# Performance work log

Measured on AMD Instinct MI355X. Metric: run time of the kernel, lower is better.

The kernel has to match this reference:

```python
import jax, jax.numpy as jnp
import numpy as np

B, T, E, D = 256, 128, 256, 256


def setup_inputs() -> dict:
    key = jax.random.key(0)
    ks = jax.random.split(key, 8)
    x = jax.random.normal(ks[0], (B, T, E), dtype=jnp.float32)
    # torch default Linear init: U(-1/sqrt(fan_in), 1/sqrt(fan_in)) for proj layers;
    # TreeLSTMCell.reset_parameters uses U(-1/sqrt(hidden), 1/sqrt(hidden)).
    se = 1.0 / np.sqrt(E)
    sd = 1.0 / np.sqrt(D)
    Wp = jax.random.uniform(ks[1], (E, D), jnp.float32, -se, se)
    bp = jax.random.uniform(ks[2], (D,), jnp.float32, -se, se)
    Wg = jax.random.uniform(ks[3], (E, D), jnp.float32, -se, se)
    bg = jax.random.uniform(ks[4], (D,), jnp.float32, -se, se)
    Wr = jax.random.uniform(ks[5], (2 * D, 5 * D), jnp.float32, -sd, sd)
    br = jax.random.uniform(ks[6], (5 * D,), jnp.float32, -sd, sd)
    # Valid shift-reduce sequence (right-branching): S, then (S, R) x (T-1) -> length 2T-1.
    pat = np.zeros(2 * T - 1, dtype=np.int32)
    pat[2::2] = 1  # REDUCE at odd stack-growth points
    transitions = jnp.asarray(np.broadcast_to(pat[:, None], (2 * T - 1, B)).copy())
    return {"x": x, "Wp": Wp, "bp": bp, "Wg": Wg, "bg": bg,
            "Wr": Wr, "br": br, "transitions": transitions}


def reference(x, Wp, bp, Wg, bg, Wr, br, transitions):
    Bx, Tx, _ = x.shape
    Dh = Wp.shape[1]
    # leaf transformation: c = Wx+b ; h = sigmoid(gate) * tanh(c)
    c_buf = x @ Wp + bp                                   # [B, T, D]
    h_buf = jax.nn.sigmoid(x @ Wg + bg) * jnp.tanh(c_buf)  # [B, T, D]
    buffers = jnp.concatenate([h_buf, c_buf], axis=-1)    # [B, T, 2D]

    stack0 = jnp.zeros((Bx, Tx, 2 * Dh), x.dtype)
    ptr0 = jnp.zeros((Bx,), jnp.int32)          # stack pointer (next free slot)
    bptr0 = jnp.full((Bx,), Tx - 1, jnp.int32)  # buffer pop index (pops from end)
    bidx = jnp.arange(Bx)

    def step(carry, trans_t):
        stack, ptr, bptr = carry
        is_shift = trans_t == 0
        shift_val = buffers[bidx, bptr]                       # [B, 2D]
        r = stack[bidx, jnp.maximum(ptr - 1, 0)]              # right child (top)
        l = stack[bidx, jnp.maximum(ptr - 2, 0)]              # left child
        h_l, c_l = l[:, :Dh], l[:, Dh:]
        h_r, c_r = r[:, :Dh], r[:, Dh:]
        proj = jnp.concatenate([h_l, h_r], axis=-1) @ Wr + br  # [B, 5D]
        i, f_l, f_r, g, o = jnp.split(proj, 5, axis=-1)
        c = (jax.nn.sigmoid(i) * jnp.tanh(g)
             + jax.nn.sigmoid(f_l) * c_l
             + jax.nn.sigmoid(f_r) * c_r)
        h = jax.nn.sigmoid(o) * jnp.tanh(c)
        red = jnp.concatenate([h, c], axis=-1)                # [B, 2D]
        pos = jnp.where(is_shift, ptr, jnp.maximum(ptr - 2, 0))
        val = jnp.where(is_shift[:, None], shift_val, red)
        stack = stack.at[bidx, pos].set(val)
        ptr = ptr + jnp.where(is_shift, jnp.int32(1), jnp.int32(-1))
        bptr = bptr - is_shift.astype(jnp.int32)
        return (stack, ptr, bptr), None

    (stack, ptr, _), _ = jax.lax.scan(step, (stack0, ptr0, bptr0), transitions)
    final = stack[bidx, jnp.maximum(ptr - 1, 0)][:, :Dh]  # root h states [B, D]
    return final
```

## Files before the change

kernel.cpp:

```cpp
#include <hip/hip_runtime.h>


typedef unsigned int u32;
typedef short s16x8 __attribute__((ext_vector_type(8)));
typedef float f32x4 __attribute__((ext_vector_type(4)));

#define MFMA16(a, b, c) __builtin_amdgcn_mfma_f32_16x16x32_bf16((a), (b), (c), 0, 0, 0)

static __device__ __forceinline__ unsigned short f2bf(float x) {
  u32 u = __builtin_bit_cast(u32, x);
  u += 0x7fffu + ((u >> 16) & 1u);
  return (unsigned short)(u >> 16);
}
static __device__ __forceinline__ float bf2f(unsigned short s) {
  u32 u = ((u32)s) << 16;
  return __builtin_bit_cast(float, u);
}
static __device__ __forceinline__ u32 packhl(float x) {
  unsigned short hi = f2bf(x);
  unsigned short lo = f2bf(x - bf2f(hi));
  return ((u32)hi << 16) | (u32)lo;
}
static __device__ __forceinline__ float unpackhl(u32 p) {
  return bf2f((unsigned short)(p >> 16)) + bf2f((unsigned short)(p & 0xffffu));
}
static __device__ __forceinline__ void unpack8(uint4 a, uint4 b, s16x8 &hi, s16x8 &lo) {
  hi[0] = (short)(a.x >> 16); lo[0] = (short)a.x;
  hi[1] = (short)(a.y >> 16); lo[1] = (short)a.y;
  hi[2] = (short)(a.z >> 16); lo[2] = (short)a.z;
  hi[3] = (short)(a.w >> 16); lo[3] = (short)a.w;
  hi[4] = (short)(b.x >> 16); lo[4] = (short)b.x;
  hi[5] = (short)(b.y >> 16); lo[5] = (short)b.y;
  hi[6] = (short)(b.z >> 16); lo[6] = (short)b.z;
  hi[7] = (short)(b.w >> 16); lo[7] = (short)b.w;
}
static __device__ __forceinline__ void split8(const float *w, s16x8 &hi, s16x8 &lo) {
#pragma unroll
  for (int i = 0; i < 8; i++) {
    unsigned short h = f2bf(w[i]);
    hi[i] = (short)h;
    lo[i] = (short)f2bf(w[i] - bf2f(h));
  }
}
static __device__ __forceinline__ float sigm(float x) { return 1.0f / (1.0f + expf(-x)); }
static __device__ __forceinline__ int vslot(int code) {
  return (code & 15) * 2 + ((code >> 4) & 1);
}

__global__ __launch_bounds__(256) void pack_kernel(
    const float *__restrict__ Wp, const float *__restrict__ Wg,
    const float *__restrict__ Wr, const float *__restrict__ x,
    u32 *__restrict__ Wpg_t, u32 *__restrict__ Wr_t, u32 *__restrict__ xpk,
    u32 *__restrict__ vstkH, float *__restrict__ vstkC, int do_x) {
  int tid = blockIdx.x * 256 + threadIdx.x;
  if (tid < 131072) {
    int isg = tid >= 65536;
    int s = tid & 65535;
    int k = s >> 8, col = s & 255;
    float v = isg ? Wg[s] : Wp[s];
    Wpg_t[(isg ? 256 + col : col) * 256 + k] = packhl(v);
  }
  if (tid < 655360) {
    int k = tid / 1280;
    int col = tid - k * 1280;
    Wr_t[col * 512 + k] = packhl(Wr[tid]);
  }
  if (tid < 65536) {
    vstkH[31 * 65536 + tid] = 0u;
    vstkC[31 * 65536 + tid] = 0.0f;
  }
  if (do_x && tid < 8388608) xpk[tid] = packhl(x[tid]);
}

__global__ __launch_bounds__(256) void plan_kernel(
    const int *__restrict__ trans, int *__restrict__ pL, int *__restrict__ pR,
    int *__restrict__ pW, int *__restrict__ fdesc) {
  int b = threadIdx.x;
  u32 t0 = 0x9F9F9F9Fu, t1 = t0, t2 = t0, t3 = t0;
  u32 verb = 0;
  int ptr = 0, bptr = 127;

  auto get = [&](int p) -> u32 {
    u32 w = p < 8 ? (p < 4 ? t0 : t1) : (p < 12 ? t2 : t3);
    return (w >> ((p & 3) * 8)) & 0xffu;
  };
  auto set = [&](int p, u32 e) {
    u32 sh = (u32)(p & 3) * 8u;
    u32 m = ~(0xffu << sh);
    u32 nv = e << sh;
    int ws = p >> 2;
    t0 = ws == 0 ? (t0 & m) | nv : t0;
    t1 = ws == 1 ? (t1 & m) | nv : t1;
    t2 = ws == 2 ? (t2 & m) | nv : t2;
    t3 = ws == 3 ? (t3 & m) | nv : t3;
  };
  auto dostep = [&](int tr, int &l, int &r, int &w) {
    if (tr == 0) {
      int pos = min(ptr, 15);
      set(pos, (u32)(bptr & 127));
      ptr++; bptr--;
    } else {
      int pl = min(max(ptr - 2, 0), 15);
      int pr = min(max(ptr - 1, 0), 15);
      l = (int)get(pl);
      r = (int)get(pr);
      u32 v = ((verb >> pl) & 1u) ^ 1u;
      verb = (verb & ~(1u << pl)) | (v << pl);
      set(pl, 0x80u | (v << 4) | (u32)pl);
      w = pl * 2 + (int)v;
      ptr--;
    }
  };
  auto ext = [&](int e) -> int { return (e & 0x80) ? (0x8000 | (e & 0x1f)) : e; };

  for (int f = 0; f < 128; ++f) {
    int l = 0x9F, r = 0x9F, w = -1;
    dostep(trans[(2 * f) * 256 + b], l, r, w);
    if (2 * f + 1 < 255) dostep(trans[(2 * f + 1) * 256 + b], l, r, w);
    pL[f * 256 + b] = ext(l);
    pR[f * 256 + b] = ext(r);
    pW[f * 256 + b] = w;
  }
  fdesc[b] = ext((int)get(min(max(ptr - 1, 0), 15)));
}

template <int UX>
__global__ __launch_bounds__(64) void front_kernel(
    const float *__restrict__ x, const u32 *__restrict__ xpk,
    const u32 *__restrict__ Wpg, const float *__restrict__ bp,
    const float *__restrict__ bg, u32 *__restrict__ h_buf,
    float *__restrict__ c_buf) {
  const int lane = threadIdx.x;
  const int rbase = blockIdx.x * 16;
  const int y = blockIdx.y;
  const int rlo = lane & 15;
  const int khi = (lane >> 4) * 8;

  f32x4 z = {0.f, 0.f, 0.f, 0.f};
  f32x4 aP[8], aG[8];
#pragma unroll
  for (int i = 0; i < 8; i++) { aP[i] = z; aG[i] = z; }

#pragma unroll 2
  for (int kt = 0; kt < 8; ++kt) {
    int k = kt * 32 + khi;
    s16x8 Ah, Al;
    if (UX) {
      const u32 *ap = xpk + (rbase + rlo) * 256 + k;
      uint4 a0 = *(const uint4 *)ap, a1 = *(const uint4 *)(ap + 4);
      unpack8(a0, a1, Ah, Al);
    } else {
      const float *ap = x + (rbase + rlo) * 256 + k;
      float4 v0 = *(const float4 *)ap;
      float4 v1 = *(const float4 *)(ap + 4);
      float w[8] = {v0.x, v0.y, v0.z, v0.w, v1.x, v1.y, v1.z, v1.w};
      split8(w, Ah, Al);
    }
#pragma unroll
    for (int nt = 0; nt < 8; ++nt) {
      int colP = y * 128 + nt * 16 + rlo;
      {
        const u32 *wp = Wpg + colP * 256 + k;
        uint4 q0 = *(const uint4 *)wp, q1 = *(const uint4 *)(wp + 4);
        s16x8 Bh, Bl;
        unpack8(q0, q1, Bh, Bl);
        aP[nt] = MFMA16(Ah, Bh, aP[nt]);
        aP[nt] = MFMA16(Ah, Bl, aP[nt]);
        aP[nt] = MFMA16(Al, Bh, aP[nt]);
      }
      {
        const u32 *wg = Wpg + (256 + colP) * 256 + k;
        uint4 q0 = *(const uint4 *)wg, q1 = *(const uint4 *)(wg + 4);
        s16x8 Bh, Bl;
        unpack8(q0, q1, Bh, Bl);
        aG[nt] = MFMA16(Ah, Bh, aG[nt]);
        aG[nt] = MFMA16(Ah, Bl, aG[nt]);
        aG[nt] = MFMA16(Al, Bh, aG[nt]);
      }
    }
  }
#pragma unroll
  for (int nt = 0; nt < 8; ++nt) {
    int d = y * 128 + nt * 16 + rlo;
    float bpd = bp[d], bgd = bg[d];
#pragma unroll
    for (int ri = 0; ri < 4; ++ri) {
      int r = rbase + (lane >> 4) * 4 + ri;
      float cv = aP[nt][ri] + bpd;
      float gv = aG[nt][ri] + bgd;
      c_buf[r * 256 + d] = cv;
      h_buf[r * 256 + d] = packhl(sigm(gv) * tanhf(cv));
    }
  }
}

#define KSTEP_BODY(SRC, KOFF)                                                \
  {                                                                          \
    const u32 *s = (SRC) + kt * 32 + khi;                                    \
    uint4 a0 = *(const uint4 *)s, a1 = *(const uint4 *)(s + 4);              \
    s16x8 Ah, Al;                                                            \
    unpack8(a0, a1, Ah, Al);                                                 \
    int kk = (KOFF) + kt * 32 + khi;                                         \
    {                                                                        \
      const u32 *wp = Wr_t + gcol0 * 512 + kk;                               \
      uint4 q0 = *(const uint4 *)wp, q1 = *(const uint4 *)(wp + 4);          \
      s16x8 Bh, Bl;                                                          \
      unpack8(q0, q1, Bh, Bl);                                               \
      acc0 = MFMA16(Ah, Bh, acc0);                                           \
      acc0 = MFMA16(Ah, Bl, acc0);                                           \
      acc0 = MFMA16(Al, Bh, acc0);                                           \
    }                                                                        \
    {                                                                        \
      const u32 *wp = Wr_t + gcol1 * 512 + kk;                               \
      uint4 q0 = *(const uint4 *)wp, q1 = *(const uint4 *)(wp + 4);          \
      s16x8 Bh, Bl;                                                          \
      unpack8(q0, q1, Bh, Bl);                                               \
      acc1 = MFMA16(Ah, Bh, acc1);                                           \
      acc1 = MFMA16(Ah, Bl, acc1);                                           \
      acc1 = MFMA16(Al, Bh, acc1);                                           \
    }                                                                        \
    {                                                                        \
      const u32 *wp = Wr_t + gcol2 * 512 + kk;                               \
      uint4 q0 = *(const uint4 *)wp, q1 = *(const uint4 *)(wp + 4);          \
      s16x8 Bh, Bl;                                                          \
      unpack8(q0, q1, Bh, Bl);                                               \
      acc2 = MFMA16(Ah, Bh, acc2);                                           \
      acc2 = MFMA16(Ah, Bl, acc2);                                           \
      acc2 = MFMA16(Al, Bh, acc2);                                           \
    }                                                                        \
  }

__global__ __launch_bounds__(64) void ppre_kernel(
    const float *__restrict__ br, const u32 *__restrict__ Wr_t,
    const u32 *__restrict__ h_buf, const u32 *__restrict__ vzero,
    const int *__restrict__ pL, const int *__restrict__ pR,
    const int *__restrict__ pW, float *__restrict__ ppre) {
  const int c = blockIdx.x;
  const int fl = blockIdx.y >> 4;
  const int g = blockIdx.y & 15;
  const int lane = threadIdx.x;
  const int b0 = g * 16;
  const int b = b0 + (lane & 15);

  const int lc = pL[fl * 256 + b];
  const int rc = pR[fl * 256 + b];
  const int w = pW[fl * 256 + b];
  if (__ballot(w >= 0) == 0ull) return;

  const bool lbuf = (lc & 0x8000) == 0;
  const bool rbuf = (rc & 0x8000) == 0;
  const u32 *srcT = lbuf ? h_buf + (((b << 7) + (lc & 127)) << 8) : vzero + (b << 8);
  const u32 *srcB = rbuf ? h_buf + (((b << 7) + (rc & 127)) << 8) : vzero + (b << 8);
  const bool doT = __ballot(w >= 0 && lbuf) != 0ull;
  const bool doB = __ballot(w >= 0 && rbuf) != 0ull;

  const int khi = (lane >> 4) * 8;
  const int cl = lane & 15;
  const int v2c = 32 + cl;
  const int gcol0 = (cl >> 3) * 256 + c * 8 + (cl & 7);
  const int gcol1 = ((16 + cl) >> 3) * 256 + c * 8 + (cl & 7);
  const int gcol2 = (v2c < 40) ? (v2c >> 3) * 256 + c * 8 + (v2c & 7) : 0;

  f32x4 acc0 = {0.f, 0.f, 0.f, 0.f}, acc1 = acc0, acc2 = acc0;
  if (doT) {
#pragma unroll 4
    for (int kt = 0; kt < 8; ++kt) KSTEP_BODY(srcT, 0)
  }
  if (doB) {
#pragma unroll 4
    for (int kt = 0; kt < 8; ++kt) KSTEP_BODY(srcB, 256)
  }

  int wcs[4];
#pragma unroll
  for (int ri = 0; ri < 4; ++ri) wcs[ri] = __shfl(w, (lane >> 4) * 4 + ri);
  float br0 = br[gcol0], br1 = br[gcol1], br2 = br[gcol2];
  float *pr = ppre + (size_t)fl * 327680;
#pragma unroll
  for (int ri = 0; ri < 4; ++ri) {
    if (wcs[ri] >= 0) {
      int b2 = b0 + (lane >> 4) * 4 + ri;
      float *row = pr + b2 * 1280;
      row[gcol0] = acc0[ri] + br0;
      row[gcol1] = acc1[ri] + br1;
      if (v2c < 40) row[gcol2] = acc2[ri] + br2;
    }
  }
}

template <int PPRE>
__global__ __launch_bounds__(64) void step_kernel(
    const float *__restrict__ br, const u32 *__restrict__ Wr_t,
    const u32 *__restrict__ h_buf, const float *__restrict__ c_buf,
    u32 *__restrict__ vstkH, float *__restrict__ vstkC,
    const u32 *__restrict__ vzero, const int *__restrict__ pL,
    const int *__restrict__ pR, const int *__restrict__ pW,
    const float *__restrict__ ppre) {
  const int c = blockIdx.x;
  const int g = blockIdx.y;
  const int lane = threadIdx.x;
  const int b0 = g * 16;
  const int b = b0 + (lane & 15);

  const int lc = pL[b];
  const int rc = pR[b];
  const int w = pW[b];
  if (__ballot(w >= 0) == 0ull) return;

  const bool lval = (lc & 0x8000) != 0;
  const bool rval = (rc & 0x8000) != 0;
  const u32 *srcT, *srcB;
  if (PPRE) {
    srcT = lval ? vstkH + ((vslot(lc) * 256 + b) << 8) : vzero + (b << 8);
    srcB = rval ? vstkH + ((vslot(rc) * 256 + b) << 8) : vzero + (b << 8);
  } else {
    srcT = lval ? vstkH + ((vslot(lc) * 256 + b) << 8)
                : h_buf + (((b << 7) + (lc & 127)) << 8);
    srcB = rval ? vstkH + ((vslot(rc) * 256 + b) << 8)
                : h_buf + (((b << 7) + (rc & 127)) << 8);
  }
  const bool doT = PPRE ? (__ballot(w >= 0 && lval) != 0ull) : true;
  const bool doB = PPRE ? (__ballot(w >= 0 && rval) != 0ull) : true;

  const int khi = (lane >> 4) * 8;
  const int cl = lane & 15;
  const int v2c = 32 + cl;
  const int gcol0 = (cl >> 3) * 256 + c * 8 + (cl & 7);
  const int gcol1 = ((16 + cl) >> 3) * 256 + c * 8 + (cl & 7);
  const int gcol2 = (v2c < 40) ? (v2c >> 3) * 256 + c * 8 + (v2c & 7) : 0;

  f32x4 acc0 = {0.f, 0.f, 0.f, 0.f}, acc1 = acc0, acc2 = acc0;
  if (doT) {
#pragma unroll 4
    for (int kt = 0; kt < 8; ++kt) KSTEP_BODY(srcT, 0)
  }
  if (doB) {
#pragma unroll 4
    for (int kt = 0; kt < 8; ++kt) KSTEP_BODY(srcB, 256)
  }

  f32x4 flv, gv;
#pragma unroll
  for (int ri = 0; ri < 4; ++ri) {
    flv[ri] = __shfl_xor(acc0[ri], 8);
    gv[ri] = __shfl_xor(acc1[ri], 8);
  }
  int lcs[4], rcs[4], wcs[4];
#pragma unroll
  for (int ri = 0; ri < 4; ++ri) {
    int rr = (lane >> 4) * 4 + ri;
    lcs[ri] = __shfl(lc, rr);
    rcs[ri] = __shfl(rc, rr);
    wcs[ri] = __shfl(w, rr);
  }
  int colj = lane & 15;
  if (colj < 8) {
    int d = c * 8 + colj;
    float brI = 0, brFl = 0, brFr = 0, brG = 0, brO = 0;
    if (!PPRE) {
      brI = br[d]; brFl = br[256 + d]; brFr = br[512 + d];
      brG = br[768 + d]; brO = br[1024 + d];
    }
#pragma unroll
    for (int ri = 0; ri < 4; ++ri) {
      if (wcs[ri] >= 0) {
        int b2 = b0 + (lane >> 4) * 4 + ri;
        int lc2 = lcs[ri], rc2 = rcs[ri];
        float c_l = (lc2 & 0x8000)
                        ? vstkC[(vslot(lc2) * 256 + b2) * 256 + d]
                        : c_buf[(b2 * 128 + (lc2 & 127)) * 256 + d];
        float c_r = (rc2 & 0x8000)
                        ? vstkC[(vslot(rc2) * 256 + b2) * 256 + d]
                        : c_buf[(b2 * 128 + (rc2 & 127)) * 256 + d];
        float pI, pFl, pFr, pG, pO;
        if (PPRE) {
          const float *row = ppre + (size_t)b2 * 1280;
          pI = row[d]; pFl = row[256 + d]; pFr = row[512 + d];
          pG = row[768 + d]; pO = row[1024 + d];
        } else {
          pI = brI; pFl = brFl; pFr = brFr; pG = brG; pO = brO;
        }
        float ii = acc0[ri] + pI;
        float fl = flv[ri] + pFl;
        float fr = acc1[ri] + pFr;
        float gg = gv[ri] + pG;
        float oo = acc2[ri] + pO;
        float cv = sigm(ii) * tanhf(gg) + sigm(fl) * c_l + sigm(fr) * c_r;
        float hv = sigm(oo) * tanhf(cv);
        int sidx = wcs[ri];
        vstkH[(sidx * 256 + b2) * 256 + d] = packhl(hv);
        vstkC[(sidx * 256 + b2) * 256 + d] = cv;
      }
    }
  }
}

__global__ __launch_bounds__(256) void out_kernel(
    const int *__restrict__ fdesc, const u32 *__restrict__ h_buf,
    const u32 *__restrict__ vstkH, float *__restrict__ out) {
  int tid = blockIdx.x * 256 + threadIdx.x;
  int b = tid >> 8, d = tid & 255;
  int code = fdesc[b];
  u32 hv = (code & 0x8000)
               ? vstkH[(vslot(code) * 256 + b) * 256 + d]
               : h_buf[(b * 128 + (code & 127)) * 256 + d];
  out[tid] = unpackhl(hv);
}

extern "C" void kernel_launch(void *const *d_in, const int *in_sizes, int n_in,
                              void *d_out, int out_size, void *d_ws, size_t ws_size,
                              hipStream_t stream) {
  const float *x = (const float *)d_in[0];
  const float *Wp = (const float *)d_in[1];
  const float *bp = (const float *)d_in[2];
  const float *Wg = (const float *)d_in[3];
  const float *bg = (const float *)d_in[4];
  const float *Wr = (const float *)d_in[5];
  const float *br = (const float *)d_in[6];
  const int *trans = (const int *)d_in[7];
  float *out = (float *)d_out;

  char *ws = (char *)d_ws;
  u32 *Wr_t = (u32 *)(ws);
  u32 *Wpg = (u32 *)(ws + 2621440);
  u32 *h_buf = (u32 *)(ws + 3145728);
  float *c_buf = (float *)(ws + 36700160);
  u32 *vstkH = (u32 *)(ws + 70254592);
  float *vstkC = (float *)(ws + 78643200);
  int *planL = (int *)(ws + 87031808);
  int *planR = (int *)(ws + 87162880);
  int *planW = (int *)(ws + 87293952);
  int *fdesc = (int *)(ws + 87425024);
  const u32 *vzero = vstkH + 31 * 65536;

  const size_t fixed_end = 87426048;
  const size_t slotB = 1310720;
  const size_t xpkB = 33554432;
  size_t avail = ws_size > fixed_end ? ws_size - fixed_end : 0;
  size_t tail = fixed_end;
  int use_xpk = 0;
  if (avail >= xpkB + 4 * slotB) { use_xpk = 1; tail += xpkB; avail -= xpkB; }
  u32 *xpk = (u32 *)(ws + fixed_end);
  int R = (int)(avail / slotB);
  if (R > 32) R = 32;
  R &= ~1;
  int use_ppre = (R >= 2);
  int C = use_ppre ? R / 2 : 0;
  float *ppre = (float *)(ws + tail);

  pack_kernel<<<use_xpk ? 32768 : 2560, 256, 0, stream>>>(
      Wp, Wg, Wr, x, Wpg, Wr_t, xpk, vstkH, vstkC, use_xpk);
  plan_kernel<<<1, 256, 0, stream>>>(trans, planL, planR, planW, fdesc);
  if (use_xpk)
    front_kernel<1><<<dim3(2048, 2), 64, 0, stream>>>(x, xpk, Wpg, bp, bg, h_buf, c_buf);
  else
    front_kernel<0><<<dim3(2048, 2), 64, 0, stream>>>(x, xpk, Wpg, bp, bg, h_buf, c_buf);

  if (use_ppre) {
    int nch = (128 + C - 1) / C;
    auto pre = [&](int k) {
      int f0 = k * C;
      int Ck = min(C, 128 - f0);
      ppre_kernel<<<dim3(32, Ck * 16), 64, 0, stream>>>(
          br, Wr_t, h_buf, vzero, planL + f0 * 256, planR + f0 * 256,
          planW + f0 * 256, ppre + (size_t)((k & 1) * C) * 327680);
    };
    pre(0);
    if (nch > 1) pre(1);
    for (int k = 0; k < nch; ++k) {
      int f0 = k * C;
      int Ck = min(C, 128 - f0);
      for (int fl = 0; fl < Ck; ++fl) {
        int f = f0 + fl;
        step_kernel<1><<<dim3(32, 16), 64, 0, stream>>>(
            br, Wr_t, h_buf, c_buf, vstkH, vstkC, vzero, planL + f * 256,
            planR + f * 256, planW + f * 256,
            ppre + (size_t)((k & 1) * C + fl) * 327680);
      }
      if (k + 2 < nch) pre(k + 2);
    }
  } else {
    for (int f = 0; f < 128; ++f)
      step_kernel<0><<<dim3(32, 16), 64, 0, stream>>>(
          br, Wr_t, h_buf, c_buf, vstkH, vstkC, vzero, planL + f * 256,
          planR + f * 256, planW + f * 256, nullptr);
  }
  out_kernel<<<256, 256, 0, stream>>>(fdesc, h_buf, vstkH, out);
}
```

Baseline: 2.249 ms.

## Replace per-step kernel launches with persistent scan kernel using group barriers

Replaces the 128 per-step kernel launches (plus chunked precompute kernels) with one persistent kernel of 512 workgroups. Each group of 32 workgroups sharing a batch slice synchronizes through an atomic counter barrier between steps. The ppre precompute of buffer-leaf projections and the packed-x path are removed, and the front kernel is split into 4 column groups instead of 2. This trades launch overhead and ppre traffic for spin-barrier latency and recomputing buffer-side matmuls inside the serial loop. It also relies on all 512 workgroups being co-resident to avoid deadlock.

```diff
diff --git a/kernel.cpp b/kernel.cpp
--- a/kernel.cpp
+++ b/kernel.cpp
@@ -4,6 +4,8 @@
 typedef unsigned int u32;
 typedef short s16x8 __attribute__((ext_vector_type(8)));
 typedef float f32x4 __attribute__((ext_vector_type(4)));
+
+#define NPAIR 128
 
 #define MFMA16(a, b, c) __builtin_amdgcn_mfma_f32_16x16x32_bf16((a), (b), (c), 0, 0, 0)
 
@@ -49,9 +51,9 @@
 
 __global__ __launch_bounds__(256) void pack_kernel(
     const float *__restrict__ Wp, const float *__restrict__ Wg,
-    const float *__restrict__ Wr, const float *__restrict__ x,
-    u32 *__restrict__ Wpg_t, u32 *__restrict__ Wr_t, u32 *__restrict__ xpk,
-    u32 *__restrict__ vstkH, float *__restrict__ vstkC, int do_x) {
+    const float *__restrict__ Wr, u32 *__restrict__ Wpg_t,
+    u32 *__restrict__ Wr_t, u32 *__restrict__ vstkH, float *__restrict__ vstkC,
+    u32 *__restrict__ bar, int do_bar) {
   int tid = blockIdx.x * 256 + threadIdx.x;
   if (tid < 131072) {
     int isg = tid >= 65536;
@@ -69,67 +71,73 @@
     vstkH[31 * 65536 + tid] = 0u;
     vstkC[31 * 65536 + tid] = 0.0f;
   }
-  if (do_x && tid < 8388608) xpk[tid] = packhl(x[tid]);
-}
+  if (do_bar && tid < 512) bar[tid] = 0u;
+}
+
+#define PGET(p, dst)                                                         \
+  {                                                                          \
+    u32 wsel = ((p) & 8) ? (((p) & 4) ? t3 : t2) : (((p) & 4) ? t1 : t0);    \
+    dst = (int)((wsel >> (((p) & 3) * 8)) & 0xffu);                          \
+  }
+#define PSET(p, e)                                                           \
+  {                                                                          \
+    u32 sh_ = (u32)((p) & 3) * 8u;                                           \
+    u32 m_ = ~(0xffu << sh_);                                                \
+    u32 nv_ = ((u32)(e)) << sh_;                                             \
+    int w_ = (p) >> 2;                                                       \
+    t0 = (w_ == 0) ? ((t0 & m_) | nv_) : t0;                                 \
+    t1 = (w_ == 1) ? ((t1 & m_) | nv_) : t1;                                 \
+    t2 = (w_ == 2) ? ((t2 & m_) | nv_) : t2;                                 \
+    t3 = (w_ == 3) ? ((t3 & m_) | nv_) : t3;                                 \
+  }
+#define PDOSTEP(tr, l, r, w)                                                 \
+  {                                                                          \
+    if ((tr) == 0) {                                                         \
+      int pos_ = min(ptr, 15);                                               \
+      PSET(pos_, (u32)(bptr & 127));                                         \
+      ptr++;                                                                 \
+      bptr--;                                                                \
+    } else {                                                                 \
+      int pl_ = min(max(ptr - 2, 0), 15);                                    \
+      int pr_ = min(max(ptr - 1, 0), 15);                                    \
+      PGET(pl_, l);                                                          \
+      PGET(pr_, r);                                                          \
+      u32 v_ = ((verb >> pl_) & 1u) ^ 1u;                                    \
+      verb = (verb & ~(1u << pl_)) | (v_ << pl_);                            \
+      PSET(pl_, 0x80u | (v_ << 4) | (u32)pl_);                               \
+      w = pl_ * 2 + (int)v_;                                                 \
+      ptr--;                                                                 \
+    }                                                                        \
+  }
 
 __global__ __launch_bounds__(256) void plan_kernel(
     const int *__restrict__ trans, int *__restrict__ pL, int *__restrict__ pR,
     int *__restrict__ pW, int *__restrict__ fdesc) {
   int b = threadIdx.x;
-  u32 t0 = 0x9F9F9F9Fu, t1 = t0, t2 = t0, t3 = t0;
+  u32 t0 = 0x9F9F9F9Fu, t1 = 0x9F9F9F9Fu, t2 = 0x9F9F9F9Fu, t3 = 0x9F9F9F9Fu;
   u32 verb = 0;
   int ptr = 0, bptr = 127;
 
-  auto get = [&](int p) -> u32 {
-    u32 w = p < 8 ? (p < 4 ? t0 : t1) : (p < 12 ? t2 : t3);
-    return (w >> ((p & 3) * 8)) & 0xffu;
-  };
-  auto set = [&](int p, u32 e) {
-    u32 sh = (u32)(p & 3) * 8u;
-    u32 m = ~(0xffu << sh);
-    u32 nv = e << sh;
-    int ws = p >> 2;
-    t0 = ws == 0 ? (t0 & m) | nv : t0;
-    t1 = ws == 1 ? (t1 & m) | nv : t1;
-    t2 = ws == 2 ? (t2 & m) | nv : t2;
-    t3 = ws == 3 ? (t3 & m) | nv : t3;
-  };
-  auto dostep = [&](int tr, int &l, int &r, int &w) {
-    if (tr == 0) {
-      int pos = min(ptr, 15);
-      set(pos, (u32)(bptr & 127));
-      ptr++; bptr--;
-    } else {
-      int pl = min(max(ptr - 2, 0), 15);
-      int pr = min(max(ptr - 1, 0), 15);
-      l = (int)get(pl);
-      r = (int)get(pr);
-      u32 v = ((verb >> pl) & 1u) ^ 1u;
-      verb = (verb & ~(1u << pl)) | (v << pl);
-      set(pl, 0x80u | (v << 4) | (u32)pl);
-      w = pl * 2 + (int)v;
-      ptr--;
-    }
-  };
-  auto ext = [&](int e) -> int { return (e & 0x80) ? (0x8000 | (e & 0x1f)) : e; };
-
-  for (int f = 0; f < 128; ++f) {
+  for (int f = 0; f < NPAIR; ++f) {
+    int trA = trans[(2 * f) * 256 + b];
+    int trB = (2 * f + 1 < 255) ? trans[(2 * f + 1) * 256 + b] : -1;
     int l = 0x9F, r = 0x9F, w = -1;
-    dostep(trans[(2 * f) * 256 + b], l, r, w);
-    if (2 * f + 1 < 255) dostep(trans[(2 * f + 1) * 256 + b], l, r, w);
-    pL[f * 256 + b] = ext(l);
-    pR[f * 256 + b] = ext(r);
+    PDOSTEP(trA, l, r, w);
+    if (trB >= 0) PDOSTEP(trB, l, r, w);
+    pL[f * 256 + b] = (l & 0x80) ? (0x8000 | (l & 0x1f)) : l;
+    pR[f * 256 + b] = (r & 0x80) ? (0x8000 | (r & 0x1f)) : r;
     pW[f * 256 + b] = w;
   }
-  fdesc[b] = ext((int)get(min(max(ptr - 1, 0), 15)));
-}
-
-template <int UX>
+  int pf = min(max(ptr - 1, 0), 15);
+  int fd;
+  PGET(pf, fd);
+  fdesc[b] = (fd & 0x80) ? (0x8000 | (fd & 0x1f)) : fd;
+}
+
 __global__ __launch_bounds__(64) void front_kernel(
-    const float *__restrict__ x, const u32 *__restrict__ xpk,
-    const u32 *__restrict__ Wpg, const float *__restrict__ bp,
-    const float *__restrict__ bg, u32 *__restrict__ h_buf,
-    float *__restrict__ c_buf) {
+    const float *__restrict__ x, const u32 *__restrict__ Wpg,
+    const float *__restrict__ bp, const float *__restrict__ bg,
+    u32 *__restrict__ h_buf, float *__restrict__ c_buf) {
   const int lane = threadIdx.x;
   const int rbase = blockIdx.x * 16;
   const int y = blockIdx.y;
@@ -137,19 +145,15 @@
   const int khi = (lane >> 4) * 8;
 
   f32x4 z = {0.f, 0.f, 0.f, 0.f};
-  f32x4 aP[8], aG[8];
-#pragma unroll
-  for (int i = 0; i < 8; i++) { aP[i] = z; aG[i] = z; }
+  f32x4 aP[4], aG[4];
+#pragma unroll
+  for (int i = 0; i < 4; i++) { aP[i] = z; aG[i] = z; }
 
 #pragma unroll 2
   for (int kt = 0; kt < 8; ++kt) {
     int k = kt * 32 + khi;
     s16x8 Ah, Al;
-    if (UX) {
-      const u32 *ap = xpk + (rbase + rlo) * 256 + k;
-      uint4 a0 = *(const uint4 *)ap, a1 = *(const uint4 *)(ap + 4);
-      unpack8(a0, a1, Ah, Al);
-    } else {
+    {
       const float *ap = x + (rbase + rlo) * 256 + k;
       float4 v0 = *(const float4 *)ap;
       float4 v1 = *(const float4 *)(ap + 4);
@@ -157,8 +161,8 @@
       split8(w, Ah, Al);
     }
 #pragma unroll
-    for (int nt = 0; nt < 8; ++nt) {
-      int colP = y * 128 + nt * 16 + rlo;
+    for (int nt = 0; nt < 4; ++nt) {
+      int colP = y * 64 + nt * 16 + rlo;
       {
         const u32 *wp = Wpg + colP * 256 + k;
         uint4 q0 = *(const uint4 *)wp, q1 = *(const uint4 *)(wp + 4);
@@ -180,8 +184,8 @@
     }
   }
 #pragma unroll
-  for (int nt = 0; nt < 8; ++nt) {
-    int d = y * 128 + nt * 16 + rlo;
+  for (int nt = 0; nt < 4; ++nt) {
+    int d = y * 64 + nt * 16 + rlo;
     float bpd = bp[d], bgd = bg[d];
 #pragma unroll
     for (int ri = 0; ri < 4; ++ri) {
@@ -230,29 +234,18 @@
     }                                                                        \
   }
 
-__global__ __launch_bounds__(64) void ppre_kernel(
-    const float *__restrict__ br, const u32 *__restrict__ Wr_t,
-    const u32 *__restrict__ h_buf, const u32 *__restrict__ vzero,
-    const int *__restrict__ pL, const int *__restrict__ pR,
-    const int *__restrict__ pW, float *__restrict__ ppre) {
-  const int c = blockIdx.x;
-  const int fl = blockIdx.y >> 4;
-  const int g = blockIdx.y & 15;
-  const int lane = threadIdx.x;
-  const int b0 = g * 16;
+static __device__ __forceinline__ void step_body(
+    int c, int b0, int lane, const float *__restrict__ br,
+    const u32 *__restrict__ Wr_t, const u32 *__restrict__ h_buf,
+    const float *__restrict__ c_buf, u32 *__restrict__ vstkH,
+    float *__restrict__ vstkC, int lc, int rc, int w) {
   const int b = b0 + (lane & 15);
-
-  const int lc = pL[fl * 256 + b];
-  const int rc = pR[fl * 256 + b];
-  const int w = pW[fl * 256 + b];
-  if (__ballot(w >= 0) == 0ull) return;
-
-  const bool lbuf = (lc & 0x8000) == 0;
-  const bool rbuf = (rc & 0x8000) == 0;
-  const u32 *srcT = lbuf ? h_buf + (((b << 7) + (lc & 127)) << 8) : vzero + (b << 8);
-  const u32 *srcB = rbuf ? h_buf + (((b << 7) + (rc & 127)) << 8) : vzero + (b << 8);
-  const bool doT = __ballot(w >= 0 && lbuf) != 0ull;
-  const bool doB = __ballot(w >= 0 && rbuf) != 0ull;
+  const bool lval = (lc & 0x8000) != 0;
+  const bool rval = (rc & 0x8000) != 0;
+  const u32 *srcT = lval ? vstkH + ((vslot(lc) * 256 + b) << 8)
+                         : h_buf + (((b << 7) + (lc & 127)) << 8);
+  const u32 *srcB = rval ? vstkH + ((vslot(rc) * 256 + b) << 8)
+                         : h_buf + (((b << 7) + (rc & 127)) << 8);
 
   const int khi = (lane >> 4) * 8;
   const int cl = lane & 15;
@@ -262,82 +255,10 @@
   const int gcol2 = (v2c < 40) ? (v2c >> 3) * 256 + c * 8 + (v2c & 7) : 0;
 
   f32x4 acc0 = {0.f, 0.f, 0.f, 0.f}, acc1 = acc0, acc2 = acc0;
-  if (doT) {
 #pragma unroll 4
-    for (int kt = 0; kt < 8; ++kt) KSTEP_BODY(srcT, 0)
-  }
-  if (doB) {
+  for (int kt = 0; kt < 8; ++kt) KSTEP_BODY(srcT, 0)
 #pragma unroll 4
-    for (int kt = 0; kt < 8; ++kt) KSTEP_BODY(srcB, 256)
-  }
-
-  int wcs[4];
-#pragma unroll
-  for (int ri = 0; ri < 4; ++ri) wcs[ri] = __shfl(w, (lane >> 4) * 4 + ri);
-  float br0 = br[gcol0], br1 = br[gcol1], br2 = br[gcol2];
-  float *pr = ppre + (size_t)fl * 327680;
-#pragma unroll
-  for (int ri = 0; ri < 4; ++ri) {
-    if (wcs[ri] >= 0) {
-      int b2 = b0 + (lane >> 4) * 4 + ri;
-      float *row = pr + b2 * 1280;
-      row[gcol0] = acc0[ri] + br0;
-      row[gcol1] = acc1[ri] + br1;
-      if (v2c < 40) row[gcol2] = acc2[ri] + br2;
-    }
-  }
-}
-
-template <int PPRE>
-__global__ __launch_bounds__(64) void step_kernel(
-    const float *__restrict__ br, const u32 *__restrict__ Wr_t,
-    const u32 *__restrict__ h_buf, const float *__restrict__ c_buf,
-    u32 *__restrict__ vstkH, float *__restrict__ vstkC,
-    const u32 *__restrict__ vzero, const int *__restrict__ pL,
-    const int *__restrict__ pR, const int *__restrict__ pW,
-    const float *__restrict__ ppre) {
-  const int c = blockIdx.x;
-  const int g = blockIdx.y;
-  const int lane = threadIdx.x;
-  const int b0 = g * 16;
-  const int b = b0 + (lane & 15);
-
-  const int lc = pL[b];
-  const int rc = pR[b];
-  const int w = pW[b];
-  if (__ballot(w >= 0) == 0ull) return;
-
-  const bool lval = (lc & 0x8000) != 0;
-  const bool rval = (rc & 0x8000) != 0;
-  const u32 *srcT, *srcB;
-  if (PPRE) {
-    srcT = lval ? vstkH + ((vslot(lc) * 256 + b) << 8) : vzero + (b << 8);
-    srcB = rval ? vstkH + ((vslot(rc) * 256 + b) << 8) : vzero + (b << 8);
-  } else {
-    srcT = lval ? vstkH + ((vslot(lc) * 256 + b) << 8)
-                : h_buf + (((b << 7) + (lc & 127)) << 8);
-    srcB = rval ? vstkH + ((vslot(rc) * 256 + b) << 8)
-                : h_buf + (((b << 7) + (rc & 127)) << 8);
-  }
-  const bool doT = PPRE ? (__ballot(w >= 0 && lval) != 0ull) : true;
-  const bool doB = PPRE ? (__ballot(w >= 0 && rval) != 0ull) : true;
-
-  const int khi = (lane >> 4) * 8;
-  const int cl = lane & 15;
-  const int v2c = 32 + cl;
-  const int gcol0 = (cl >> 3) * 256 + c * 8 + (cl & 7);
-  const int gcol1 = ((16 + cl) >> 3) * 256 + c * 8 + (cl & 7);
-  const int gcol2 = (v2c < 40) ? (v2c >> 3) * 256 + c * 8 + (v2c & 7) : 0;
-
-  f32x4 acc0 = {0.f, 0.f, 0.f, 0.f}, acc1 = acc0, acc2 = acc0;
-  if (doT) {
-#pragma unroll 4
-    for (int kt = 0; kt < 8; ++kt) KSTEP_BODY(srcT, 0)
-  }
-  if (doB) {
-#pragma unroll 4
-    for (int kt = 0; kt < 8; ++kt) KSTEP_BODY(srcB, 256)
-  }
+  for (int kt = 0; kt < 8; ++kt) KSTEP_BODY(srcB, 256)
 
   f32x4 flv, gv;
 #pragma unroll
@@ -356,11 +277,8 @@
   int colj = lane & 15;
   if (colj < 8) {
     int d = c * 8 + colj;
-    float brI = 0, brFl = 0, brFr = 0, brG = 0, brO = 0;
-    if (!PPRE) {
-      brI = br[d]; brFl = br[256 + d]; brFr = br[512 + d];
-      brG = br[768 + d]; brO = br[1024 + d];
-    }
+    float brI = br[d], brFl = br[256 + d], brFr = br[512 + d];
+    float brG = br[768 + d], brO = br[1024 + d];
 #pragma unroll
     for (int ri = 0; ri < 4; ++ri) {
       if (wcs[ri] >= 0) {
@@ -372,19 +290,11 @@
         float c_r = (rc2 & 0x8000)
                         ? vstkC[(vslot(rc2) * 256 + b2) * 256 + d]
                         : c_buf[(b2 * 128 + (rc2 & 127)) * 256 + d];
-        float pI, pFl, pFr, pG, pO;
-        if (PPRE) {
-          const float *row = ppre + (size_t)b2 * 1280;
-          pI = row[d]; pFl = row[256 + d]; pFr = row[512 + d];
-          pG = row[768 + d]; pO = row[1024 + d];
-        } else {
-          pI = brI; pFl = brFl; pFr = brFr; pG = brG; pO = brO;
-        }
-        float ii = acc0[ri] + pI;
-        float fl = flv[ri] + pFl;
-        float fr = acc1[ri] + pFr;
-        float gg = gv[ri] + pG;
-        float oo = acc2[ri] + pO;
+        float ii = acc0[ri] + brI;
+        float fl = flv[ri] + brFl;
+        float fr = acc1[ri] + brFr;
+        float gg = gv[ri] + brG;
+        float oo = acc2[ri] + brO;
         float cv = sigm(ii) * tanhf(gg) + sigm(fl) * c_l + sigm(fr) * c_r;
         float hv = sigm(oo) * tanhf(cv);
         int sidx = wcs[ri];
@@ -393,6 +303,67 @@
       }
     }
   }
+}
+
+__global__ __launch_bounds__(64) void scan_kernel(
+    const float *__restrict__ br, const u32 *__restrict__ Wr_t,
+    const u32 *__restrict__ h_buf, const float *__restrict__ c_buf,
+    u32 *__restrict__ vstkH, float *__restrict__ vstkC,
+    const int *__restrict__ pL, const int *__restrict__ pR,
+    const int *__restrict__ pW, u32 *bar) {
+  const int c = blockIdx.x;
+  const int g = blockIdx.y;
+  const int lane = threadIdx.x;
+  const int b0 = g * 16;
+  u32 *mybar = bar + g * 32;
+
+  for (int f = 0; f < NPAIR; ++f) {
+    int lc = 0, rc = 0, w = -1;
+    if (lane < 16) {
+      int b = b0 + lane;
+      lc = pL[f * 256 + b];
+      rc = pR[f * 256 + b];
+      w = pW[f * 256 + b];
+    }
+    lc = __shfl(lc, lane & 15);
+    rc = __shfl(rc, lane & 15);
+    w = __shfl(w, lane & 15);
+
+    if (__ballot(w >= 0) != 0ull)
+      step_body(c, b0, lane, br, Wr_t, h_buf, c_buf, vstkH, vstkC, lc, rc, w);
+
+    __threadfence();
+    if (lane == 0) {
+      __hip_atomic_fetch_add(mybar, 1u, __ATOMIC_RELEASE, __HIP_MEMORY_SCOPE_AGENT);
+      u32 tgt = 32u * (u32)(f + 1);
+      while (__hip_atomic_load(mybar, __ATOMIC_ACQUIRE, __HIP_MEMORY_SCOPE_AGENT) < tgt)
+        __builtin_amdgcn_s_sleep(1);
+    }
+    __threadfence();
+  }
+}
+
+__global__ __launch_bounds__(64) void step_kernel(
+    const float *__restrict__ br, const u32 *__restrict__ Wr_t,
+    const u32 *__restrict__ h_buf, const float *__restrict__ c_buf,
+    u32 *__restrict__ vstkH, float *__restrict__ vstkC,
+    const int *__restrict__ pL, const int *__restrict__ pR,
+    const int *__restrict__ pW) {
+  const int c = blockIdx.x;
+  const int b0 = blockIdx.y * 16;
+  const int lane = threadIdx.x;
+  int lc = 0, rc = 0, w = -1;
+  if (lane < 16) {
+    int b = b0 + lane;
+    lc = pL[b];
+    rc = pR[b];
+    w = pW[b];
+  }
+  lc = __shfl(lc, lane & 15);
+  rc = __shfl(rc, lane & 15);
+  w = __shfl(w, lane & 15);
+  if (__ballot(w >= 0) == 0ull) return;
+  step_body(c, b0, lane, br, Wr_t, h_buf, c_buf, vstkH, vstkC, lc, rc, w);
 }
 
 __global__ __launch_bounds__(256) void out_kernel(
@@ -431,59 +402,23 @@
   int *planR = (int *)(ws + 87162880);
   int *planW = (int *)(ws + 87293952);
   int *fdesc = (int *)(ws + 87425024);
-  const u32 *vzero = vstkH + 31 * 65536;
-
-  const size_t fixed_end = 87426048;
-  const size_t slotB = 1310720;
-  const size_t xpkB = 33554432;
-  size_t avail = ws_size > fixed_end ? ws_size - fixed_end : 0;
-  size_t tail = fixed_end;
-  int use_xpk = 0;
-  if (avail >= xpkB + 4 * slotB) { use_xpk = 1; tail += xpkB; avail -= xpkB; }
-  u32 *xpk = (u32 *)(ws + fixed_end);
-  int R = (int)(avail / slotB);
-  if (R > 32) R = 32;
-  R &= ~1;
-  int use_ppre = (R >= 2);
-  int C = use_ppre ? R / 2 : 0;
-  float *ppre = (float *)(ws + tail);
-
-  pack_kernel<<<use_xpk ? 32768 : 2560, 256, 0, stream>>>(
-      Wp, Wg, Wr, x, Wpg, Wr_t, xpk, vstkH, vstkC, use_xpk);
+  u32 *bar = (u32 *)(ws + 87426048);
+
+  const int use_scan = (ws_size >= (size_t)87426048 + 2048) ? 1 : 0;
+
+  pack_kernel<<<2560, 256, 0, stream>>>(Wp, Wg, Wr, Wpg, Wr_t, vstkH, vstkC,
+                                        bar, use_scan);
   plan_kernel<<<1, 256, 0, stream>>>(trans, planL, planR, planW, fdesc);
-  if (use_xpk)
-    front_kernel<1><<<dim3(2048, 2), 64, 0, stream>>>(x, xpk, Wpg, bp, bg, h_buf, c_buf);
-  else
-    front_kernel<0><<<dim3(2048, 2), 64, 0, stream>>>(x, xpk, Wpg, bp, bg, h_buf, c_buf);
-
-  if (use_ppre) {
-    int nch = (128 + C - 1) / C;
-    auto pre = [&](int k) {
-      int f0 = k * C;
-      int Ck = min(C, 128 - f0);
-      ppre_kernel<<<dim3(32, Ck * 16), 64, 0, stream>>>(
-          br, Wr_t, h_buf, vzero, planL + f0 * 256, planR + f0 * 256,
-          planW + f0 * 256, ppre + (size_t)((k & 1) * C) * 327680);
-    };
-    pre(0);
-    if (nch > 1) pre(1);
-    for (int k = 0; k < nch; ++k) {
-      int f0 = k * C;
-      int Ck = min(C, 128 - f0);
-      for (int fl = 0; fl < Ck; ++fl) {
-        int f = f0 + fl;
-        step_kernel<1><<<dim3(32, 16), 64, 0, stream>>>(
-            br, Wr_t, h_buf, c_buf, vstkH, vstkC, vzero, planL + f * 256,
-            planR + f * 256, planW + f * 256,
-            ppre + (size_t)((k & 1) * C + fl) * 327680);
-      }
-      if (k + 2 < nch) pre(k + 2);
-    }
+  front_kernel<<<dim3(2048, 4), 64, 0, stream>>>(x, Wpg, bp, bg, h_buf, c_buf);
+
+  if (use_scan) {
+    scan_kernel<<<dim3(32, 16), 64, 0, stream>>>(br, Wr_t, h_buf, c_buf, vstkH,
+                                                 vstkC, planL, planR, planW, bar);
   } else {
-    for (int f = 0; f < 128; ++f)
-      step_kernel<0><<<dim3(32, 16), 64, 0, stream>>>(
-          br, Wr_t, h_buf, c_buf, vstkH, vstkC, vzero, planL + f * 256,
-          planR + f * 256, planW + f * 256, nullptr);
+    for (int f = 0; f < NPAIR; ++f)
+      step_kernel<<<dim3(32, 16), 64, 0, stream>>>(
+          br, Wr_t, h_buf, c_buf, vstkH, vstkC, planL + f * 256,
+          planR + f * 256, planW + f * 256);
   }
   out_kernel<<<256, 256, 0, stream>>>(fdesc, h_buf, vstkH, out);
 }
```

Result: slower. 6.336 ms (+181.7%).
